# Kernel tuning notes

Measured on AMD Instinct MI355X. Metric: run time of the kernel, lower is better.

## Reference

```python
import jax, jax.numpy as jnp
import numpy as np

NUM_TOKENS = 100
D_MODEL = 256
NUM_RBF = 50
CUTOFF = 12.0


def setup_inputs() -> dict:
    key = jax.random.key(0)
    k1, k2, k3, k4, k5 = jax.random.split(key, 5)
    B, N = 16, 512
    atomic_numbers = jax.random.randint(k1, (B, N), 0, NUM_TOKENS)
    # scale positions so pairwise distances span [0, cutoff]
    positions = jax.random.normal(k2, (B, N, 3), dtype=jnp.float32) * 3.0
    token_emb = jax.random.normal(k3, (NUM_TOKENS, D_MODEL), dtype=jnp.float32) * 0.02
    proj_w = jax.random.normal(k4, (NUM_RBF, D_MODEL), dtype=jnp.float32) * (1.0 / np.sqrt(NUM_RBF))
    proj_b = jax.random.normal(k5, (D_MODEL,), dtype=jnp.float32) * 0.01
    return {"atomic_numbers": atomic_numbers, "positions": positions,
            "token_emb": token_emb, "proj_w": proj_w, "proj_b": proj_b}


def reference(atomic_numbers, positions, token_emb, proj_w, proj_b):
    # pairwise distances [B, N, N]
    diff = positions[:, :, None, :] - positions[:, None, :, :]
    dist = jnp.sqrt(jnp.sum(diff * diff, axis=-1) + 1e-8)
    # fixed Gaussian RBF expansion [B, N, N, K]
    centers = jnp.linspace(0.0, CUTOFF, NUM_RBF, dtype=jnp.float32)
    width = (centers[1] - centers[0]) * 2.0
    rbf = jnp.exp(-((dist[..., None] - centers) ** 2) / (width * width))
    # mean over neighbor axis -> [B, N, K]
    rbf_mean = jnp.mean(rbf, axis=2)
    rbf_embeddings = rbf_mean @ proj_w + proj_b  # [B, N, d_model]
    token_embeddings = token_emb[atomic_numbers]  # [B, N, d_model]
    return token_embeddings + rbf_embeddings
```

## Files before the change

kernel.cpp:

```cpp
#include <hip/hip_runtime.h>

#define S_C     2.45229158f
#define TWO_DS  1.20112241f
#define TEN_D   6.00560980f
#define E5_1 6.73794700e-3f
#define E5_2 4.53999298e-5f
#define E5_3 3.05902321e-7f
#define E5_4 2.06115362e-9f

typedef float v2f __attribute__((ext_vector_type(2)));

__device__ __forceinline__ float fast_exp2(float x) {
#if __has_builtin(__builtin_amdgcn_exp2f)
    return __builtin_amdgcn_exp2f(x);
#else
    float r;
    asm("v_exp_f32 %0, %1" : "=v"(r) : "v"(x));
    return r;
#endif
}
__device__ __forceinline__ float fast_sqrt(float x) {
#if __has_builtin(__builtin_amdgcn_sqrtf)
    return __builtin_amdgcn_sqrtf(x);
#else
    return sqrtf(x);
#endif
}

template <bool FUSED>
__global__ __launch_bounds__(256, 5)
void rbf_mean_kernel(const float* __restrict__ pos,
                     float* __restrict__ meanout,
                     const int* __restrict__ an,
                     const float* __restrict__ te,
                     const float* __restrict__ pw,
                     const float* __restrict__ pb,
                     float* __restrict__ out)
{
    __shared__ v2f red2[4][32 * 25];

    const int w    = threadIdx.x >> 6;
    const int lane = threadIdx.x & 63;
    const int row  = blockIdx.x * 4 + w;
    const int b    = row >> 9;
    const int i    = row & 511;

    const float* posb = pos + (size_t)b * 1536;

    const int i3 = __builtin_amdgcn_readfirstlane(3 * i);
    const float pix = posb[i3 + 0];
    const float piy = posb[i3 + 1];
    const float piz = posb[i3 + 2];

    v2f acc[25];
#pragma unroll
    for (int m = 0; m < 25; ++m) acc[m] = (v2f){0.0f, 0.0f};

    const int l3 = lane * 3;
#pragma unroll 2
    for (int jj = 0; jj < 8; ++jj) {
        const float* pj = posb + jj * 192 + l3;
        const float dx = pix - pj[0];
        const float dy = piy - pj[1];
        const float dz = piz - pj[2];
        const float d2 = fmaf(dx, dx, fmaf(dy, dy, fmaf(dz, dz, 1e-8f)));
        float dS = fast_sqrt(d2) * S_C;
        dS = fminf(dS, 42.0f);
        const float Ap = fast_exp2(dS * TWO_DS);

#pragma unroll
        for (int c = 0; c < 5; ++c) {
            const float u  = dS - (float)c * TEN_D;
            const float t0 = fast_exp2(-(u * u));
            const float Ac  = (c == 0) ? Ap :
                              (c == 1) ? Ap * E5_1 :
                              (c == 2) ? Ap * E5_2 :
                              (c == 3) ? Ap * E5_3 : Ap * E5_4;
            const float Ac2 = Ac * Ac;
            v2f g = {t0, t0 * Ac};
            acc[5 * c + 0] += g;
            const v2f M = {Ac2, Ac2};
#pragma unroll
            for (int t = 1; t < 5; ++t) {
                g = g * M;
                acc[5 * c + t] += g;
            }
        }
    }

    {
        const v2f QP[5] = {{1.0f,            0.778800783f},
                           {0.367879441f,    0.105399225f},
                           {1.83156389e-2f,  1.93045414e-3f},
                           {1.23409804e-4f,  4.78511739e-6f},
                           {1.12535175e-7f,  1.60522806e-9f}};
#pragma unroll
        for (int m = 0; m < 25; ++m) acc[m] = acc[m] * QP[m % 5];
    }

#pragma unroll
    for (int m = 0; m < 25; ++m) {
        const float lx = __shfl_xor(acc[m].x, 1);
        const float ly = __shfl_xor(acc[m].y, 1);
        acc[m] += (v2f){lx, ly};
    }
    if ((lane & 1) == 0) {
        v2f* myrow = &red2[w][(lane >> 1) * 25];
#pragma unroll
        for (int m = 0; m < 25; ++m) myrow[m] = acc[m];
    }
    __syncthreads();

    float meanv = 0.0f;
    if (lane < 50) {
        const float* col = (const float*)&red2[w][0] + lane;
        float s0 = 0.f, s1 = 0.f, s2 = 0.f, s3 = 0.f;
#pragma unroll
        for (int r = 0; r < 32; r += 4) {
            s0 += col[(r + 0) * 50];
            s1 += col[(r + 1) * 50];
            s2 += col[(r + 2) * 50];
            s3 += col[(r + 3) * 50];
        }
        meanv = ((s0 + s1) + (s2 + s3)) * (1.0f / 512.0f);
    }

    if constexpr (!FUSED) {
        if (lane < 50) meanout[(size_t)row * 50 + lane] = meanv;
    } else {
        __shared__ float ms[4][52];
        if (lane < 50) ms[w][lane] = meanv;
        __syncthreads();

        const int tok = an[row];
        float4 o = reinterpret_cast<const float4*>(pb)[lane];
        const float4 t = reinterpret_cast<const float4*>(te + (size_t)tok * 256)[lane];
        o.x += t.x; o.y += t.y; o.z += t.z; o.w += t.w;
#pragma unroll
        for (int k = 0; k < 50; ++k) {
            const float mk = ms[w][k];
            const float4 w4 = reinterpret_cast<const float4*>(pw + k * 256)[lane];
            o.x = fmaf(mk, w4.x, o.x);
            o.y = fmaf(mk, w4.y, o.y);
            o.z = fmaf(mk, w4.z, o.z);
            o.w = fmaf(mk, w4.w, o.w);
        }
        reinterpret_cast<float4*>(out)[(size_t)row * 64 + lane] = o;
    }
}

__global__ __launch_bounds__(256)
void proj_kernel(const float* __restrict__ mean,
                 const int* __restrict__ an,
                 const float* __restrict__ te,
                 const float* __restrict__ pw,
                 const float* __restrict__ pb,
                 float* __restrict__ out)
{
    const int w    = threadIdx.x >> 6;
    const int lane = threadIdx.x & 63;
    int wid = blockIdx.x * 4 + w;
    wid = __builtin_amdgcn_readfirstlane(wid);
    const int row0 = wid * 4;

    const float4 bias = reinterpret_cast<const float4*>(pb)[lane];
    float4 o[4];
#pragma unroll
    for (int r = 0; r < 4; ++r) {
        const int tok = an[row0 + r];
        const float4 t = reinterpret_cast<const float4*>(te + (size_t)tok * 256)[lane];
        o[r].x = bias.x + t.x; o[r].y = bias.y + t.y;
        o[r].z = bias.z + t.z; o[r].w = bias.w + t.w;
    }
#pragma unroll
    for (int k = 0; k < 50; ++k) {
        const float4 w4 = reinterpret_cast<const float4*>(pw + (size_t)k * 256)[lane];
#pragma unroll
        for (int r = 0; r < 4; ++r) {
            const float mk = mean[(size_t)(row0 + r) * 50 + k];
            o[r].x = fmaf(mk, w4.x, o[r].x);
            o[r].y = fmaf(mk, w4.y, o[r].y);
            o[r].z = fmaf(mk, w4.z, o[r].z);
            o[r].w = fmaf(mk, w4.w, o[r].w);
        }
    }
#pragma unroll
    for (int r = 0; r < 4; ++r)
        reinterpret_cast<float4*>(out)[(size_t)(row0 + r) * 64 + lane] = o[r];
}

extern "C" void kernel_launch(void* const* d_in, const int* in_sizes, int n_in,
                              void* d_out, int out_size, void* d_ws, size_t ws_size,
                              hipStream_t stream)
{
    const int*   an  = (const int*)  d_in[0];
    const float* pos = (const float*)d_in[1];
    const float* te  = (const float*)d_in[2];
    const float* pw  = (const float*)d_in[3];
    const float* pb  = (const float*)d_in[4];
    float* out = (float*)d_out;

    const size_t mean_bytes = (size_t)8192 * 50 * sizeof(float);
    if (ws_size >= mean_bytes) {
        float* mean = (float*)d_ws;
        rbf_mean_kernel<false><<<2048, 256, 0, stream>>>(pos, mean, nullptr, nullptr,
                                                         nullptr, nullptr, nullptr);
        proj_kernel<<<512, 256, 0, stream>>>(mean, an, te, pw, pb, out);
    } else {
        rbf_mean_kernel<true><<<2048, 256, 0, stream>>>(pos, nullptr, an, te, pw, pb, out);
    }
}
```

Before: 29.66 us.

## Split RBF accumulation into two passes with DPP quad reduction

Splits the 25 paired accumulators into two passes over neighbours (3 and 2 centre groups), which recomputes distances and sqrt/exp per pass to lower live register count. It replaces the pairwise shuffle with a DPP quad-sum so only every fourth lane writes partial sums, halving the LDS reduction rows. It drops the block barriers, relying on each wave touching only its own LDS slice, and doubles rows per wave in the projection kernel. The trade is extra distance and exp work in exchange for lower register pressure and a cheaper reduction, plus a reliance on intra-wave LDS ordering without a barrier.

```diff
diff --git a/kernel.cpp b/kernel.cpp
--- a/kernel.cpp
+++ b/kernel.cpp
@@ -3,10 +3,6 @@
 #define S_C     2.45229158f
 #define TWO_DS  1.20112241f
 #define TEN_D   6.00560980f
-#define E5_1 6.73794700e-3f
-#define E5_2 4.53999298e-5f
-#define E5_3 3.05902321e-7f
-#define E5_4 2.06115362e-9f
 
 typedef float v2f __attribute__((ext_vector_type(2)));
 
@@ -27,37 +23,27 @@
 #endif
 }
 
-template <bool FUSED>
-__global__ __launch_bounds__(256, 5)
-void rbf_mean_kernel(const float* __restrict__ pos,
-                     float* __restrict__ meanout,
-                     const int* __restrict__ an,
-                     const float* __restrict__ te,
-                     const float* __restrict__ pw,
-                     const float* __restrict__ pb,
-                     float* __restrict__ out)
-{
-    __shared__ v2f red2[4][32 * 25];
-
-    const int w    = threadIdx.x >> 6;
-    const int lane = threadIdx.x & 63;
-    const int row  = blockIdx.x * 4 + w;
-    const int b    = row >> 9;
-    const int i    = row & 511;
-
-    const float* posb = pos + (size_t)b * 1536;
-
-    const int i3 = __builtin_amdgcn_readfirstlane(3 * i);
-    const float pix = posb[i3 + 0];
-    const float piy = posb[i3 + 1];
-    const float piz = posb[i3 + 2];
-
-    v2f acc[25];
-#pragma unroll
-    for (int m = 0; m < 25; ++m) acc[m] = (v2f){0.0f, 0.0f};
-
-    const int l3 = lane * 3;
-#pragma unroll 2
+__device__ __forceinline__ float quad_sum(float x) {
+    int a = __builtin_amdgcn_update_dpp(0, __float_as_int(x), 0xB1, 0xF, 0xF, true);
+    x += __int_as_float(a);
+    int b = __builtin_amdgcn_update_dpp(0, __float_as_int(x), 0x4E, 0xF, 0xF, true);
+    x += __int_as_float(b);
+    return x;
+}
+
+__constant__ const float E5tab[5] = {1.0f, 6.73794700e-3f, 4.53999298e-5f,
+                                     3.05902321e-7f, 2.06115362e-9f};
+
+template <int C0, int NC>
+__device__ __forceinline__ void rbf_pass(const float* __restrict__ posb, int l3,
+                                         float pix, float piy, float piz,
+                                         v2f* __restrict__ red_row, bool writer)
+{
+    v2f acc[NC * 5];
+#pragma unroll
+    for (int m = 0; m < NC * 5; ++m) acc[m] = (v2f){0.0f, 0.0f};
+
+#pragma unroll
     for (int jj = 0; jj < 8; ++jj) {
         const float* pj = posb + jj * 192 + l3;
         const float dx = pix - pj[0];
@@ -69,54 +55,76 @@
         const float Ap = fast_exp2(dS * TWO_DS);
 
 #pragma unroll
-        for (int c = 0; c < 5; ++c) {
+        for (int ci = 0; ci < NC; ++ci) {
+            constexpr int dummy = 0; (void)dummy;
+            const int c = C0 + ci;
             const float u  = dS - (float)c * TEN_D;
             const float t0 = fast_exp2(-(u * u));
-            const float Ac  = (c == 0) ? Ap :
-                              (c == 1) ? Ap * E5_1 :
-                              (c == 2) ? Ap * E5_2 :
-                              (c == 3) ? Ap * E5_3 : Ap * E5_4;
+            const float Ac  = Ap * E5tab[c];
             const float Ac2 = Ac * Ac;
             v2f g = {t0, t0 * Ac};
-            acc[5 * c + 0] += g;
+            acc[ci * 5 + 0] += g;
             const v2f M = {Ac2, Ac2};
 #pragma unroll
             for (int t = 1; t < 5; ++t) {
                 g = g * M;
-                acc[5 * c + t] += g;
+                acc[ci * 5 + t] += g;
             }
         }
     }
 
-    {
-        const v2f QP[5] = {{1.0f,            0.778800783f},
-                           {0.367879441f,    0.105399225f},
-                           {1.83156389e-2f,  1.93045414e-3f},
-                           {1.23409804e-4f,  4.78511739e-6f},
-                           {1.12535175e-7f,  1.60522806e-9f}};
-#pragma unroll
-        for (int m = 0; m < 25; ++m) acc[m] = acc[m] * QP[m % 5];
-    }
-
-#pragma unroll
-    for (int m = 0; m < 25; ++m) {
-        const float lx = __shfl_xor(acc[m].x, 1);
-        const float ly = __shfl_xor(acc[m].y, 1);
-        acc[m] += (v2f){lx, ly};
-    }
-    if ((lane & 1) == 0) {
-        v2f* myrow = &red2[w][(lane >> 1) * 25];
-#pragma unroll
-        for (int m = 0; m < 25; ++m) myrow[m] = acc[m];
-    }
-    __syncthreads();
+    const v2f QP[5] = {{1.0f,            0.778800783f},
+                       {0.367879441f,    0.105399225f},
+                       {1.83156389e-2f,  1.93045414e-3f},
+                       {1.23409804e-4f,  4.78511739e-6f},
+                       {1.12535175e-7f,  1.60522806e-9f}};
+#pragma unroll
+    for (int m = 0; m < NC * 5; ++m) {
+        v2f v = acc[m] * QP[m % 5];
+        v.x = quad_sum(v.x);
+        v.y = quad_sum(v.y);
+        if (writer) red_row[C0 * 5 + m] = v;
+    }
+}
+
+template <bool FUSED>
+__global__ __launch_bounds__(256)
+void rbf_mean_kernel(const float* __restrict__ pos,
+                     float* __restrict__ meanout,
+                     const int* __restrict__ an,
+                     const float* __restrict__ te,
+                     const float* __restrict__ pw,
+                     const float* __restrict__ pb,
+                     float* __restrict__ out)
+{
+    __shared__ v2f red2[4][16 * 25];
+
+    const int w    = threadIdx.x >> 6;
+    const int lane = threadIdx.x & 63;
+    const int row  = blockIdx.x * 4 + w;
+    const int b    = row >> 9;
+    const int i    = row & 511;
+
+    const float* posb = pos + (size_t)b * 1536;
+
+    const int i3 = __builtin_amdgcn_readfirstlane(3 * i);
+    const float pix = posb[i3 + 0];
+    const float piy = posb[i3 + 1];
+    const float piz = posb[i3 + 2];
+
+    const int  l3     = lane * 3;
+    const bool writer = (lane & 3) == 0;
+    v2f* red_row = &red2[w][(lane >> 2) * 25];
+
+    rbf_pass<0, 3>(posb, l3, pix, piy, piz, red_row, writer);
+    rbf_pass<3, 2>(posb, l3, pix, piy, piz, red_row, writer);
 
     float meanv = 0.0f;
     if (lane < 50) {
         const float* col = (const float*)&red2[w][0] + lane;
         float s0 = 0.f, s1 = 0.f, s2 = 0.f, s3 = 0.f;
 #pragma unroll
-        for (int r = 0; r < 32; r += 4) {
+        for (int r = 0; r < 16; r += 4) {
             s0 += col[(r + 0) * 50];
             s1 += col[(r + 1) * 50];
             s2 += col[(r + 2) * 50];
@@ -130,8 +138,6 @@
     } else {
         __shared__ float ms[4][52];
         if (lane < 50) ms[w][lane] = meanv;
-        __syncthreads();
-
         const int tok = an[row];
         float4 o = reinterpret_cast<const float4*>(pb)[lane];
         const float4 t = reinterpret_cast<const float4*>(te + (size_t)tok * 256)[lane];
@@ -161,12 +167,12 @@
     const int lane = threadIdx.x & 63;
     int wid = blockIdx.x * 4 + w;
     wid = __builtin_amdgcn_readfirstlane(wid);
-    const int row0 = wid * 4;
+    const int row0 = wid * 8;
 
     const float4 bias = reinterpret_cast<const float4*>(pb)[lane];
-    float4 o[4];
-#pragma unroll
-    for (int r = 0; r < 4; ++r) {
+    float4 o[8];
+#pragma unroll
+    for (int r = 0; r < 8; ++r) {
         const int tok = an[row0 + r];
         const float4 t = reinterpret_cast<const float4*>(te + (size_t)tok * 256)[lane];
         o[r].x = bias.x + t.x; o[r].y = bias.y + t.y;
@@ -176,7 +182,7 @@
     for (int k = 0; k < 50; ++k) {
         const float4 w4 = reinterpret_cast<const float4*>(pw + (size_t)k * 256)[lane];
 #pragma unroll
-        for (int r = 0; r < 4; ++r) {
+        for (int r = 0; r < 8; ++r) {
             const float mk = mean[(size_t)(row0 + r) * 50 + k];
             o[r].x = fmaf(mk, w4.x, o[r].x);
             o[r].y = fmaf(mk, w4.y, o[r].y);
@@ -185,7 +191,7 @@
         }
     }
 #pragma unroll
-    for (int r = 0; r < 4; ++r)
+    for (int r = 0; r < 8; ++r)
         reinterpret_cast<float4*>(out)[(size_t)(row0 + r) * 64 + lane] = o[r];
 }
 
@@ -205,7 +211,7 @@
         float* mean = (float*)d_ws;
         rbf_mean_kernel<false><<<2048, 256, 0, stream>>>(pos, mean, nullptr, nullptr,
                                                          nullptr, nullptr, nullptr);
-        proj_kernel<<<512, 256, 0, stream>>>(mean, an, te, pw, pb, out);
+        proj_kernel<<<256, 256, 0, stream>>>(mean, an, te, pw, pb, out);
     } else {
         rbf_mean_kernel<true><<<2048, 256, 0, stream>>>(pos, nullptr, an, te, pw, pb, out);
     }
```

Result: slower. 33.46 us (+12.8%).
